# Performance work log

Measured on AMD Instinct MI355X. Metric: run time of the kernel, lower is better.

## Reference

```python
import jax, jax.numpy as jnp
import numpy as np

N = 50000
E = 800000
IN_C = 128
HID = 64
HEADS = 4
OUT_C = 1
NEG_SLOPE = 0.2  # PyG GATConv default


def setup_inputs() -> dict:
    key = jax.random.key(0)
    ks = jax.random.split(key, 12)
    s = 1.0 / np.sqrt(IN_C)
    s2 = 1.0 / np.sqrt(HEADS * HID)
    return {
        "x": jax.random.normal(ks[0], (N, IN_C), jnp.float32),
        "edge_index": jax.random.randint(ks[1], (2, E), 0, N, jnp.int64),
        # layer 1 params (heads=HEADS, concat=True)
        "W1": jax.random.normal(ks[2], (IN_C, HEADS * HID), jnp.float32) * s,
        "att_src1": jax.random.normal(ks[3], (HEADS, HID), jnp.float32) * s,
        "att_dst1": jax.random.normal(ks[4], (HEADS, HID), jnp.float32) * s,
        "b1": jnp.zeros((HEADS * HID,), jnp.float32),
        # layer 2 params (heads=1, concat=False)
        "W2": jax.random.normal(ks[5], (HEADS * HID, OUT_C), jnp.float32) * s2,
        "att_src2": jax.random.normal(ks[6], (1, OUT_C), jnp.float32) * s2,
        "att_dst2": jax.random.normal(ks[7], (1, OUT_C), jnp.float32) * s2,
        "b2": jnp.zeros((OUT_C,), jnp.float32),
    }


def _gat_layer(x, src, dst, W, att_src, att_dst, b, concat):
    heads, out_c = att_src.shape
    h = (x @ W).reshape(-1, heads, out_c)          # [N, H, F]
    # per-node attention scores, gathered per edge (scalars, cheap)
    s_src = jnp.einsum('nhf,hf->nh', h, att_src)   # [N, H]
    s_dst = jnp.einsum('nhf,hf->nh', h, att_dst)
    e = jax.nn.leaky_relu(s_src[src] + s_dst[dst], NEG_SLOPE)  # [E, H]
    # segment softmax over edges sharing a destination
    m = jax.ops.segment_max(e, dst, num_segments=N)            # [N, H]
    m = jnp.where(jnp.isfinite(m), m, 0.0)
    ex = jnp.exp(e - m[dst])
    denom = jax.ops.segment_sum(ex, dst, num_segments=N)       # [N, H]
    alpha = ex / denom[dst]                                    # [E, H]
    # weighted scatter-aggregate of source features
    agg = jax.ops.segment_sum(alpha[:, :, None] * h[src], dst, num_segments=N)  # [N, H, F]
    out = agg.reshape(-1, heads * out_c) if concat else agg.mean(axis=1)
    return out + b


def reference(x, edge_index, W1, att_src1, att_dst1, b1, W2, att_src2, att_dst2, b2):
    # PyG GATConv default: add self loops
    loop = jnp.arange(N, dtype=edge_index.dtype)
    src = jnp.concatenate([edge_index[0], loop])
    dst = jnp.concatenate([edge_index[1], loop])
    h = _gat_layer(x, src, dst, W1, att_src1, att_dst1, b1, concat=True)
    h = jax.nn.elu(h)
    return _gat_layer(h, src, dst, W2, att_src2, att_dst2, b2, concat=False)
```

## Files before the change

### kernel.cpp

```cpp
#include <hip/hip_runtime.h>
#include <math.h>

#define NN 50000
#define EE 800000
#define ETOT 850000
#define NEG 0.2f
#define CAP 64
#define NBLK 782
#define ECHK 3321
#define NSLC 6250

typedef unsigned short ushort_t;
typedef __attribute__((ext_vector_type(8))) short bf16x8;
typedef __attribute__((ext_vector_type(4))) float f32x4;

__device__ __forceinline__ unsigned f2bf(float f) {
    unsigned u = __float_as_uint(f);
    return (u + 0x7FFFu + ((u >> 16) & 1u)) >> 16;
}
__device__ __forceinline__ unsigned cvtpk(float lo, float hi) {
    unsigned r;
    asm("v_cvt_pk_bf16_f32 %0, %1, %2" : "=v"(r) : "v"(lo), "v"(hi));
    return r;
}
__device__ __forceinline__ float blo(unsigned u) { return __uint_as_float(u << 16); }
__device__ __forceinline__ float bhi(unsigned u) { return __uint_as_float(u & 0xffff0000u); }

__device__ __forceinline__ int load_idx(const void* ei, int f64, long long pos) {
    return f64 ? (int)((const long long*)ei)[pos] : ((const int*)ei)[pos];
}

__global__ __launch_bounds__(256) void k_prep(const float* __restrict__ W,
                                              const float* __restrict__ b1,
                                              const float* __restrict__ W2,
                                              const void* ei,
                                              ushort_t* __restrict__ Wf,
                                              float* __restrict__ b1q,
                                              float* __restrict__ W2q,
                                              int* __restrict__ flag,
                                              int* __restrict__ cursor) {
    int bid = blockIdx.x, t = threadIdx.x;
    if (bid < 128) {
        int idx = bid * 256 + t;
        int e = idx & 7, l = (idx >> 3) & 63, ct = (idx >> 9) & 15, kt = idx >> 13;
        int k = kt * 32 + (l >> 4) * 8 + e;
        int col = ct * 16 + (l & 15);
        Wf[idx] = (ushort_t)f2bf(W[k * 256 + col]);
    } else if (bid == 128) {
        if (t < 64) {
            int c = t;
            int hl = c >> 1, sub = c & 1, head = c >> 4, lrr = c & 15;
#pragma unroll
            for (int kk = 0; kk < 4; ++kk) {
                b1q[hl * 8 + sub * 4 + kk] = b1[head * 64 + lrr + 16 * kk];
                W2q[hl * 8 + sub * 4 + kk] = W2[head * 64 + lrr + 16 * kk];
            }
        } else if (t == 64) {
            const long long* p = (const long long*)ei;
            int ok = 1;
            for (int i = 0; i < 64; ++i) {
                long long v = p[i];
                if (v < 0 || v >= NN) ok = 0;
            }
            *flag = ok;
        }
    } else {
        int idx = (bid - 129) * 256 + t;
        if (idx < NN / 4) ((int4*)cursor)[idx] = make_int4(0, 0, 0, 0);
    }
}

__global__ __launch_bounds__(256) void k_main(
    const float* __restrict__ x, const ushort_t* __restrict__ Wf,
    const float* __restrict__ aS, const float* __restrict__ aD,
    const void* ei, const int* __restrict__ flag,
    int* cursor, ushort_t* __restrict__ esrc,
    uint2* __restrict__ h1c, float* __restrict__ sS, float* __restrict__ sD) {
    __shared__ ushort_t xs[64][144];
    int bid = blockIdx.x, t = threadIdx.x;
    if (bid >= NBLK) {
        int s = bid & 7;
        int c = (bid - NBLK) >> 3;
        int e = c * 256 + t;
        if (e >= ETOT) return;
        int f = *flag;
        int dst = (e < EE) ? load_idx(ei, f, (long long)EE + e) : (e - EE);
        if ((unsigned)(dst - s * NSLC) < (unsigned)NSLC) {
            int src = (e < EE) ? load_idx(ei, f, e) : dst;
            int pos = atomicAdd(&cursor[dst], 1);
            if (pos < CAP) esrc[dst * CAP + pos] = (ushort_t)src;
        }
        return;
    }
    int wid = t >> 6, l = t & 63;
    int lg = l >> 4, lr = l & 15;
    int r0 = bid * 64;
    int c0 = wid * 64;
    for (int i = t; i < 1024; i += 256) {
        int row = i >> 4, c = i & 15;
        int gr = r0 + row;
        if (gr >= NN) gr = NN - 1;
        const float4* p = (const float4*)(x + (size_t)gr * 128 + c * 8);
        float4 a = p[0], b = p[1];
        uint4 v;
        v.x = cvtpk(a.x, a.y);
        v.y = cvtpk(a.z, a.w);
        v.z = cvtpk(b.x, b.y);
        v.w = cvtpk(b.z, b.w);
        *(uint4*)&xs[row][c * 8] = v;
    }
    __syncthreads();
    const bf16x8* Bv = (const bf16x8*)Wf;
    f32x4 acc[4][4] = {};
#pragma unroll
    for (int kt = 0; kt < 4; ++kt) {
        bf16x8 a[4];
#pragma unroll
        for (int rt = 0; rt < 4; ++rt)
            a[rt] = *(const bf16x8*)&xs[rt * 16 + lr][kt * 32 + lg * 8];
#pragma unroll
        for (int ct = 0; ct < 4; ++ct) {
            bf16x8 b = Bv[(size_t)((kt * 16 + wid * 4 + ct) * 64 + l)];
#pragma unroll
            for (int rt = 0; rt < 4; ++rt)
                acc[rt][ct] = __builtin_amdgcn_mfma_f32_16x16x32_bf16(a[rt], b, acc[rt][ct], 0, 0, 0);
        }
    }
    float aSl[4], aDl[4];
#pragma unroll
    for (int ct = 0; ct < 4; ++ct) {
        aSl[ct] = aS[c0 + ct * 16 + lr];
        aDl[ct] = aD[c0 + ct * 16 + lr];
    }
#pragma unroll
    for (int rt = 0; rt < 4; ++rt) {
#pragma unroll
        for (int q = 0; q < 4; ++q) {
            int row = r0 + rt * 16 + lg * 4 + q;
            bool ok = row < NN;
            float v0 = acc[rt][0][q], v1 = acc[rt][1][q];
            float v2 = acc[rt][2][q], v3 = acc[rt][3][q];
            float p = v0 * aSl[0] + v1 * aSl[1] + v2 * aSl[2] + v3 * aSl[3];
            float dd = v0 * aDl[0] + v1 * aDl[1] + v2 * aDl[2] + v3 * aDl[3];
            uint2 u;
            u.x = cvtpk(v0, v1);
            u.y = cvtpk(v2, v3);
            if (ok) h1c[(size_t)row * 64 + wid * 16 + lr] = u;
#pragma unroll
            for (int k = 8; k >= 1; k >>= 1) {
                p += __shfl_xor(p, k, 64);
                dd += __shfl_xor(dd, k, 64);
            }
            if (ok && lr == 0) {
                sS[row * 4 + wid] = p;
                sD[row * 4 + wid] = dd;
            }
        }
    }
}

__global__ __launch_bounds__(256) void k_agg1(
    const int* __restrict__ cursor, const ushort_t* __restrict__ esrc,
    const uint4* __restrict__ h1c4, const float* __restrict__ sS,
    const float* __restrict__ sD, const float* __restrict__ b1q,
    const float* __restrict__ W2q, float* __restrict__ g) {
    __shared__ float al_lds[4][CAP][4];
    __shared__ int s_lds[4][CAP];
    int wid = threadIdx.x >> 6, lane = threadIdx.x & 63;
    int n = blockIdx.x * 4 + wid;
    if (n >= NN) return;
    int d = cursor[n];
    if (d > CAP) d = CAP;
    int dp = (d + 7) & ~7;
    float4 sd = *(const float4*)(sD + (size_t)n * 4);
    float e0 = -1e30f, e1 = -1e30f, e2 = -1e30f, e3 = -1e30f;
    int s = 0;
    if (lane < d) {
        s = esrc[n * CAP + lane];
        float4 ss = *(const float4*)(sS + (size_t)s * 4);
        e0 = ss.x + sd.x; e0 = e0 > 0.f ? e0 : NEG * e0;
        e1 = ss.y + sd.y; e1 = e1 > 0.f ? e1 : NEG * e1;
        e2 = ss.z + sd.z; e2 = e2 > 0.f ? e2 : NEG * e2;
        e3 = ss.w + sd.w; e3 = e3 > 0.f ? e3 : NEG * e3;
    }
    float m0 = e0, m1 = e1, m2 = e2, m3 = e3;
#pragma unroll
    for (int k = 32; k >= 1; k >>= 1) {
        m0 = fmaxf(m0, __shfl_xor(m0, k, 64));
        m1 = fmaxf(m1, __shfl_xor(m1, k, 64));
        m2 = fmaxf(m2, __shfl_xor(m2, k, 64));
        m3 = fmaxf(m3, __shfl_xor(m3, k, 64));
    }
    float x0 = __expf(e0 - m0);
    float x1 = __expf(e1 - m1);
    float x2 = __expf(e2 - m2);
    float x3 = __expf(e3 - m3);
    float q0 = x0, q1 = x1, q2 = x2, q3 = x3;
#pragma unroll
    for (int k = 32; k >= 1; k >>= 1) {
        q0 += __shfl_xor(q0, k, 64);
        q1 += __shfl_xor(q1, k, 64);
        q2 += __shfl_xor(q2, k, 64);
        q3 += __shfl_xor(q3, k, 64);
    }
    if (lane < dp) {
        al_lds[wid][lane][0] = x0 / q0;
        al_lds[wid][lane][1] = x1 / q1;
        al_lds[wid][lane][2] = x2 / q2;
        al_lds[wid][lane][3] = x3 / q3;
        s_lds[wid][lane] = s;
    }
    __builtin_amdgcn_s_barrier();
    int hl = lane & 31, p = lane >> 5;
    int head = hl >> 3;
    float a0 = 0.f, a1 = 0.f, a2 = 0.f, a3 = 0.f;
    float a4 = 0.f, a5 = 0.f, a6 = 0.f, a7 = 0.f;
    for (int j = 0; j < dp; j += 8) {
        int i0 = j + p, i1 = j + 2 + p, i2 = j + 4 + p, i3 = j + 6 + p;
        int s0 = s_lds[wid][i0];
        int s1 = s_lds[wid][i1];
        int s2 = s_lds[wid][i2];
        int s3 = s_lds[wid][i3];
        float w0 = al_lds[wid][i0][head];
        float w1 = al_lds[wid][i1][head];
        float w2 = al_lds[wid][i2][head];
        float w3 = al_lds[wid][i3][head];
        uint4 u0 = h1c4[(size_t)s0 * 32 + hl];
        uint4 u1 = h1c4[(size_t)s1 * 32 + hl];
        uint4 u2 = h1c4[(size_t)s2 * 32 + hl];
        uint4 u3 = h1c4[(size_t)s3 * 32 + hl];
        a0 = fmaf(w0, blo(u0.x), a0); a1 = fmaf(w0, bhi(u0.x), a1);
        a2 = fmaf(w0, blo(u0.y), a2); a3 = fmaf(w0, bhi(u0.y), a3);
        a4 = fmaf(w0, blo(u0.z), a4); a5 = fmaf(w0, bhi(u0.z), a5);
        a6 = fmaf(w0, blo(u0.w), a6); a7 = fmaf(w0, bhi(u0.w), a7);
        a0 = fmaf(w1, blo(u1.x), a0); a1 = fmaf(w1, bhi(u1.x), a1);
        a2 = fmaf(w1, blo(u1.y), a2); a3 = fmaf(w1, bhi(u1.y), a3);
        a4 = fmaf(w1, blo(u1.z), a4); a5 = fmaf(w1, bhi(u1.z), a5);
        a6 = fmaf(w1, blo(u1.w), a6); a7 = fmaf(w1, bhi(u1.w), a7);
        a0 = fmaf(w2, blo(u2.x), a0); a1 = fmaf(w2, bhi(u2.x), a1);
        a2 = fmaf(w2, blo(u2.y), a2); a3 = fmaf(w2, bhi(u2.y), a3);
        a4 = fmaf(w2, blo(u2.z), a4); a5 = fmaf(w2, bhi(u2.z), a5);
        a6 = fmaf(w2, blo(u2.w), a6); a7 = fmaf(w2, bhi(u2.w), a7);
        a0 = fmaf(w3, blo(u3.x), a0); a1 = fmaf(w3, bhi(u3.x), a1);
        a2 = fmaf(w3, blo(u3.y), a2); a3 = fmaf(w3, bhi(u3.y), a3);
        a4 = fmaf(w3, blo(u3.z), a4); a5 = fmaf(w3, bhi(u3.z), a5);
        a6 = fmaf(w3, blo(u3.w), a6); a7 = fmaf(w3, bhi(u3.w), a7);
    }
    a0 += __shfl_xor(a0, 32, 64); a1 += __shfl_xor(a1, 32, 64);
    a2 += __shfl_xor(a2, 32, 64); a3 += __shfl_xor(a3, 32, 64);
    a4 += __shfl_xor(a4, 32, 64); a5 += __shfl_xor(a5, 32, 64);
    a6 += __shfl_xor(a6, 32, 64); a7 += __shfl_xor(a7, 32, 64);
    float4 bA = ((const float4*)b1q)[hl * 2];
    float4 bB = ((const float4*)b1q)[hl * 2 + 1];
    float4 wA = ((const float4*)W2q)[hl * 2];
    float4 wB = ((const float4*)W2q)[hl * 2 + 1];
    float o0 = a0 + bA.x, o1 = a1 + bA.y, o2 = a2 + bA.z, o3 = a3 + bA.w;
    float o4 = a4 + bB.x, o5 = a5 + bB.y, o6 = a6 + bB.z, o7 = a7 + bB.w;
    o0 = o0 > 0.f ? o0 : expm1f(o0);
    o1 = o1 > 0.f ? o1 : expm1f(o1);
    o2 = o2 > 0.f ? o2 : expm1f(o2);
    o3 = o3 > 0.f ? o3 : expm1f(o3);
    o4 = o4 > 0.f ? o4 : expm1f(o4);
    o5 = o5 > 0.f ? o5 : expm1f(o5);
    o6 = o6 > 0.f ? o6 : expm1f(o6);
    o7 = o7 > 0.f ? o7 : expm1f(o7);
    float part = o0 * wA.x + o1 * wA.y + o2 * wA.z + o3 * wA.w
               + o4 * wB.x + o5 * wB.y + o6 * wB.z + o7 * wB.w;
#pragma unroll
    for (int k = 16; k >= 1; k >>= 1) part += __shfl_xor(part, k, 64);
    if (lane == 0) g[n] = part;
}

__global__ __launch_bounds__(256) void k_layer2(
    const int* __restrict__ cursor, const ushort_t* __restrict__ esrc,
    const float* __restrict__ g, const float* __restrict__ aS2,
    const float* __restrict__ aD2, const float* __restrict__ b2,
    float* __restrict__ out) {
    int wid = threadIdx.x >> 6, lane = threadIdx.x & 63;
    int n = blockIdx.x * 4 + wid;
    if (n >= NN) return;
    int d = cursor[n];
    if (d > CAP) d = CAP;
    float aS = aS2[0], aD = aD2[0];
    float dn = g[n] * aD;
    float gv = 0.f, e = -1e30f;
    if (lane < d) {
        gv = g[esrc[n * CAP + lane]];
        e = gv * aS + dn;
        e = e > 0.f ? e : NEG * e;
    }
    float m = e;
#pragma unroll
    for (int k = 32; k >= 1; k >>= 1) m = fmaxf(m, __shfl_xor(m, k, 64));
    float ex = (lane < d) ? __expf(e - m) : 0.f;
    float den = ex, ws = ex * gv;
#pragma unroll
    for (int k = 32; k >= 1; k >>= 1) {
        den += __shfl_xor(den, k, 64);
        ws += __shfl_xor(ws, k, 64);
    }
    if (lane == 0) out[n] = ws / den + b2[0];
}

extern "C" void kernel_launch(void* const* d_in, const int* in_sizes, int n_in,
                              void* d_out, int out_size, void* d_ws, size_t ws_size,
                              hipStream_t stream) {
    const float* x   = (const float*)d_in[0];
    const void*  ei  = d_in[1];
    const float* W1  = (const float*)d_in[2];
    const float* aS1 = (const float*)d_in[3];
    const float* aD1 = (const float*)d_in[4];
    const float* b1  = (const float*)d_in[5];
    const float* W2  = (const float*)d_in[6];
    const float* aS2 = (const float*)d_in[7];
    const float* aD2 = (const float*)d_in[8];
    const float* b2  = (const float*)d_in[9];
    float* out = (float*)d_out;

    char* w = (char*)d_ws;
    size_t off = 0;
    auto take = [&](size_t bytes) {
        char* p = w + off;
        off = (off + bytes + 255) & ~(size_t)255;
        return p;
    };
    int*      flag   = (int*)take(4);
    int*      cursor = (int*)take((size_t)NN * 4);
    ushort_t* esrc   = (ushort_t*)take((size_t)NN * CAP * 2);
    float*    sS     = (float*)take((size_t)NN * 4 * 4);
    float*    sD     = (float*)take((size_t)NN * 4 * 4);
    float*    g      = (float*)take((size_t)NN * 4);
    void*     h1c    = take((size_t)NN * 64 * 8);
    ushort_t* Wf     = (ushort_t*)take((size_t)128 * 256 * 2);
    float*    b1q    = (float*)take((size_t)256 * 4);
    float*    W2q    = (float*)take((size_t)256 * 4);
    (void)ws_size; (void)in_sizes; (void)n_in; (void)out_size;

    k_prep<<<178, 256, 0, stream>>>(W1, b1, W2, ei, Wf, b1q, W2q, flag, cursor);
    k_main<<<NBLK + ECHK * 8, 256, 0, stream>>>(x, Wf, aS1, aD1, ei, flag,
                                                cursor, esrc, (uint2*)h1c, sS, sD);
    k_agg1<<<12500, 256, 0, stream>>>(cursor, esrc, (const uint4*)h1c, sS, sD, b1q, W2q, g);
    k_layer2<<<12500, 256, 0, stream>>>(cursor, esrc, g, aS2, aD2, b2, out);
}
```

Baseline: 140.7 us.

## Persist edge-bucketing blocks with looped chunks and use nontemporal x/h1 accesses

The edge-bucketing part of k_main now runs on a fixed 2048 blocks. Each block loops over 512-edge chunks, handling two edges per thread per iteration, so that index loads overlap and block-launch overhead drops compared with the old 26.5K single-pass blocks. The x loads and h1c stores in the GEMM part switch to nontemporal builtins to reduce cache pollution. In exchange, fewer blocks are available to hide atomic latency, and nontemporal stores of h1c could hurt reuse in k_agg1 if the data would otherwise have stayed in cache.

```diff
diff --git a/kernel.cpp b/kernel.cpp
--- a/kernel.cpp
+++ b/kernel.cpp
@@ -7,12 +7,16 @@
 #define NEG 0.2f
 #define CAP 64
 #define NBLK 782
-#define ECHK 3321
 #define NSLC 6250
+#define FGRP 256
+#define NFB (FGRP * 8)
+#define CHK2 1661
+#define FITER 7
 
 typedef unsigned short ushort_t;
 typedef __attribute__((ext_vector_type(8))) short bf16x8;
 typedef __attribute__((ext_vector_type(4))) float f32x4;
+typedef __attribute__((ext_vector_type(2))) unsigned u32x2;
 
 __device__ __forceinline__ unsigned f2bf(float f) {
     unsigned u = __float_as_uint(f);
@@ -75,20 +79,34 @@
     const float* __restrict__ aS, const float* __restrict__ aD,
     const void* ei, const int* __restrict__ flag,
     int* cursor, ushort_t* __restrict__ esrc,
-    uint2* __restrict__ h1c, float* __restrict__ sS, float* __restrict__ sD) {
+    unsigned* __restrict__ h1c, float* __restrict__ sS, float* __restrict__ sD) {
     __shared__ ushort_t xs[64][144];
     int bid = blockIdx.x, t = threadIdx.x;
     if (bid >= NBLK) {
         int s = bid & 7;
-        int c = (bid - NBLK) >> 3;
-        int e = c * 256 + t;
-        if (e >= ETOT) return;
+        int g = (bid - NBLK) >> 3;
         int f = *flag;
-        int dst = (e < EE) ? load_idx(ei, f, (long long)EE + e) : (e - EE);
-        if ((unsigned)(dst - s * NSLC) < (unsigned)NSLC) {
-            int src = (e < EE) ? load_idx(ei, f, e) : dst;
-            int pos = atomicAdd(&cursor[dst], 1);
-            if (pos < CAP) esrc[dst * CAP + pos] = (ushort_t)src;
+        int lo = s * NSLC;
+#pragma unroll
+        for (int it = 0; it < FITER; ++it) {
+            int c = g + it * FGRP;
+            if (c >= CHK2) break;
+            int eA = c * 512 + t;
+            int eB = eA + 256;
+            bool vA = eA < ETOT, vB = eB < ETOT;
+            int dstA = 0, dstB = 0;
+            if (vA) dstA = (eA < EE) ? load_idx(ei, f, (long long)EE + eA) : (eA - EE);
+            if (vB) dstB = (eB < EE) ? load_idx(ei, f, (long long)EE + eB) : (eB - EE);
+            if (vA && (unsigned)(dstA - lo) < (unsigned)NSLC) {
+                int src = (eA < EE) ? load_idx(ei, f, eA) : dstA;
+                int pos = atomicAdd(&cursor[dstA], 1);
+                if (pos < CAP) esrc[dstA * CAP + pos] = (ushort_t)src;
+            }
+            if (vB && (unsigned)(dstB - lo) < (unsigned)NSLC) {
+                int src = (eB < EE) ? load_idx(ei, f, eB) : dstB;
+                int pos = atomicAdd(&cursor[dstB], 1);
+                if (pos < CAP) esrc[dstB * CAP + pos] = (ushort_t)src;
+            }
         }
         return;
     }
@@ -100,8 +118,9 @@
         int row = i >> 4, c = i & 15;
         int gr = r0 + row;
         if (gr >= NN) gr = NN - 1;
-        const float4* p = (const float4*)(x + (size_t)gr * 128 + c * 8);
-        float4 a = p[0], b = p[1];
+        const f32x4* p = (const f32x4*)(x + (size_t)gr * 128 + c * 8);
+        f32x4 a = __builtin_nontemporal_load(p);
+        f32x4 b = __builtin_nontemporal_load(p + 1);
         uint4 v;
         v.x = cvtpk(a.x, a.y);
         v.y = cvtpk(a.z, a.w);
@@ -142,10 +161,11 @@
             float v2 = acc[rt][2][q], v3 = acc[rt][3][q];
             float p = v0 * aSl[0] + v1 * aSl[1] + v2 * aSl[2] + v3 * aSl[3];
             float dd = v0 * aDl[0] + v1 * aDl[1] + v2 * aDl[2] + v3 * aDl[3];
-            uint2 u;
+            u32x2 u;
             u.x = cvtpk(v0, v1);
             u.y = cvtpk(v2, v3);
-            if (ok) h1c[(size_t)row * 64 + wid * 16 + lr] = u;
+            if (ok) __builtin_nontemporal_store(u,
+                        (u32x2*)&h1c[((size_t)row * 64 + wid * 16 + lr) * 2]);
 #pragma unroll
             for (int k = 8; k >= 1; k >>= 1) {
                 p += __shfl_xor(p, k, 64);
@@ -337,8 +357,8 @@
     (void)ws_size; (void)in_sizes; (void)n_in; (void)out_size;
 
     k_prep<<<178, 256, 0, stream>>>(W1, b1, W2, ei, Wf, b1q, W2q, flag, cursor);
-    k_main<<<NBLK + ECHK * 8, 256, 0, stream>>>(x, Wf, aS1, aD1, ei, flag,
-                                                cursor, esrc, (uint2*)h1c, sS, sD);
+    k_main<<<NBLK + NFB, 256, 0, stream>>>(x, Wf, aS1, aD1, ei, flag,
+                                           cursor, esrc, (unsigned*)h1c, sS, sD);
     k_agg1<<<12500, 256, 0, stream>>>(cursor, esrc, (const uint4*)h1c, sS, sD, b1q, W2q, g);
     k_layer2<<<12500, 256, 0, stream>>>(cursor, esrc, g, aS2, aD2, b2, out);
 }
```

After: 143.3 us. No clear change (+1.9%).

## Pre-partition edges by destination slice before bucketing into CSR

Applied to the files above, without the earlier changes.

Adds a partition kernel that reads each edge once, packs (dst,src) into a 32-bit word and appends it to one of eight per-slice buffers using shared-memory counters and one global atomic per slice per block. Before this, each of the eight slice passes re-read the whole edge list and filtered it. The bucketing blocks in the main kernel now read only their own slice's compacted edges, which cuts redundant edge-index reads and launches far fewer blocks. The int64-versus-int32 probe moves into the partition kernel as a wave ballot. Feature loads of x become nontemporal. The cost is an extra kernel launch and a 4 MB intermediate buffer.

```diff
diff --git a/kernel.cpp b/kernel.cpp
--- a/kernel.cpp
+++ b/kernel.cpp
@@ -7,8 +7,10 @@
 #define NEG 0.2f
 #define CAP 64
 #define NBLK 782
-#define ECHK 3321
 #define NSLC 6250
+#define PBLK 416
+#define SCAPE 131072
+#define FB 440
 
 typedef unsigned short ushort_t;
 typedef __attribute__((ext_vector_type(8))) short bf16x8;
@@ -33,12 +35,11 @@
 __global__ __launch_bounds__(256) void k_prep(const float* __restrict__ W,
                                               const float* __restrict__ b1,
                                               const float* __restrict__ W2,
-                                              const void* ei,
                                               ushort_t* __restrict__ Wf,
                                               float* __restrict__ b1q,
                                               float* __restrict__ W2q,
-                                              int* __restrict__ flag,
-                                              int* __restrict__ cursor) {
+                                              int* __restrict__ cursor,
+                                              int* __restrict__ gctr) {
     int bid = blockIdx.x, t = threadIdx.x;
     if (bid < 128) {
         int idx = bid * 256 + t;
@@ -46,7 +47,9 @@
         int k = kt * 32 + (l >> 4) * 8 + e;
         int col = ct * 16 + (l & 15);
         Wf[idx] = (ushort_t)f2bf(W[k * 256 + col]);
-    } else if (bid == 128) {
+        return;
+    }
+    if (bid == 128) {
         if (t < 64) {
             int c = t;
             int hl = c >> 1, sub = c & 1, head = c >> 4, lrr = c & 15;
@@ -55,40 +58,80 @@
                 b1q[hl * 8 + sub * 4 + kk] = b1[head * 64 + lrr + 16 * kk];
                 W2q[hl * 8 + sub * 4 + kk] = W2[head * 64 + lrr + 16 * kk];
             }
-        } else if (t == 64) {
-            const long long* p = (const long long*)ei;
-            int ok = 1;
-            for (int i = 0; i < 64; ++i) {
-                long long v = p[i];
-                if (v < 0 || v >= NN) ok = 0;
-            }
-            *flag = ok;
-        }
-    } else {
-        int idx = (bid - 129) * 256 + t;
-        if (idx < NN / 4) ((int4*)cursor)[idx] = make_int4(0, 0, 0, 0);
+        } else if (t >= 64 && t < 72) {
+            gctr[t - 64] = 0;
+        }
+        return;
+    }
+    int idx = (bid - 129) * 256 + t;
+    if (idx < NN / 4) ((int4*)cursor)[idx] = make_int4(0, 0, 0, 0);
+}
+
+__global__ __launch_bounds__(256) void k_part(const void* ei,
+                                              unsigned* __restrict__ ebuf,
+                                              int* __restrict__ gctr) {
+    __shared__ int lcnt[8];
+    __shared__ int lbase[8];
+    int t = threadIdx.x;
+    long long probe = ((const long long*)ei)[t & 63];
+    unsigned long long bad = __ballot(probe < 0 || probe >= NN);
+    int f64 = (bad == 0ull);
+    if (t < 8) lcnt[t] = 0;
+    __syncthreads();
+    int e0 = blockIdx.x * 2048 + t * 8;
+    unsigned pk[8];
+    int sl[8], lpos[8];
+    bool v[8];
+#pragma unroll
+    for (int k = 0; k < 8; ++k) {
+        int e = e0 + k;
+        v[k] = e < ETOT;
+        if (v[k]) {
+            int src, dst;
+            if (e < EE) {
+                src = load_idx(ei, f64, e);
+                dst = load_idx(ei, f64, (long long)EE + e);
+            } else {
+                src = dst = e - EE;
+            }
+            pk[k] = ((unsigned)dst << 16) | (unsigned)src;
+            sl[k] = dst / NSLC;
+            lpos[k] = atomicAdd(&lcnt[sl[k]], 1);
+        }
+    }
+    __syncthreads();
+    if (t < 8) lbase[t] = atomicAdd(&gctr[t], lcnt[t]);
+    __syncthreads();
+#pragma unroll
+    for (int k = 0; k < 8; ++k) {
+        if (v[k])
+            ebuf[(size_t)sl[k] * SCAPE + lbase[sl[k]] + lpos[k]] = pk[k];
     }
 }
 
 __global__ __launch_bounds__(256) void k_main(
     const float* __restrict__ x, const ushort_t* __restrict__ Wf,
     const float* __restrict__ aS, const float* __restrict__ aD,
-    const void* ei, const int* __restrict__ flag,
+    const unsigned* __restrict__ ebuf, const int* __restrict__ gctr,
     int* cursor, ushort_t* __restrict__ esrc,
     uint2* __restrict__ h1c, float* __restrict__ sS, float* __restrict__ sD) {
     __shared__ ushort_t xs[64][144];
     int bid = blockIdx.x, t = threadIdx.x;
     if (bid >= NBLK) {
         int s = bid & 7;
-        int c = (bid - NBLK) >> 3;
-        int e = c * 256 + t;
-        if (e >= ETOT) return;
-        int f = *flag;
-        int dst = (e < EE) ? load_idx(ei, f, (long long)EE + e) : (e - EE);
-        if ((unsigned)(dst - s * NSLC) < (unsigned)NSLC) {
-            int src = (e < EE) ? load_idx(ei, f, e) : dst;
-            int pos = atomicAdd(&cursor[dst], 1);
-            if (pos < CAP) esrc[dst * CAP + pos] = (ushort_t)src;
+        int grp = (bid - NBLK) >> 3;
+        int cnt = gctr[s];
+        const unsigned* sb = ebuf + (size_t)s * SCAPE;
+        int i0 = grp * 2048 + t * 8;
+#pragma unroll
+        for (int k = 0; k < 8; ++k) {
+            int i = i0 + k;
+            if (i < cnt) {
+                unsigned u = sb[i];
+                int dst = u >> 16;
+                int pos = atomicAdd(&cursor[dst], 1);
+                if (pos < CAP) esrc[dst * CAP + pos] = (ushort_t)(u & 0xffffu);
+            }
         }
         return;
     }
@@ -100,8 +143,9 @@
         int row = i >> 4, c = i & 15;
         int gr = r0 + row;
         if (gr >= NN) gr = NN - 1;
-        const float4* p = (const float4*)(x + (size_t)gr * 128 + c * 8);
-        float4 a = p[0], b = p[1];
+        const f32x4* p = (const f32x4*)(x + (size_t)gr * 128 + c * 8);
+        f32x4 a = __builtin_nontemporal_load(p);
+        f32x4 b = __builtin_nontemporal_load(p + 1);
         uint4 v;
         v.x = cvtpk(a.x, a.y);
         v.y = cvtpk(a.z, a.w);
@@ -324,8 +368,9 @@
         off = (off + bytes + 255) & ~(size_t)255;
         return p;
     };
-    int*      flag   = (int*)take(4);
     int*      cursor = (int*)take((size_t)NN * 4);
+    int*      gctr   = (int*)take(8 * 4);
+    unsigned* ebuf   = (unsigned*)take((size_t)8 * SCAPE * 4);
     ushort_t* esrc   = (ushort_t*)take((size_t)NN * CAP * 2);
     float*    sS     = (float*)take((size_t)NN * 4 * 4);
     float*    sD     = (float*)take((size_t)NN * 4 * 4);
@@ -336,9 +381,10 @@
     float*    W2q    = (float*)take((size_t)256 * 4);
     (void)ws_size; (void)in_sizes; (void)n_in; (void)out_size;
 
-    k_prep<<<178, 256, 0, stream>>>(W1, b1, W2, ei, Wf, b1q, W2q, flag, cursor);
-    k_main<<<NBLK + ECHK * 8, 256, 0, stream>>>(x, Wf, aS1, aD1, ei, flag,
-                                                cursor, esrc, (uint2*)h1c, sS, sD);
+    k_prep<<<178, 256, 0, stream>>>(W1, b1, W2, Wf, b1q, W2q, cursor, gctr);
+    k_part<<<PBLK, 256, 0, stream>>>(ei, ebuf, gctr);
+    k_main<<<NBLK + FB, 256, 0, stream>>>(x, Wf, aS1, aD1, ebuf, gctr,
+                                          cursor, esrc, (uint2*)h1c, sS, sD);
     k_agg1<<<12500, 256, 0, stream>>>(cursor, esrc, (const uint4*)h1c, sS, sD, b1q, W2q, g);
     k_layer2<<<12500, 256, 0, stream>>>(cursor, esrc, g, aS2, aD2, b2, out);
 }
```

Result: slower. 149.6 us (+6.4%).
